# Optimization experiments

Measured on AMD Instinct MI355X. Metric: run time of the kernel, lower is better.

Reference implementation:

```python
import jax, jax.numpy as jnp
import numpy as np

N, T, D, H = 32, 512, 1024, 1024


def setup_inputs() -> dict:
    key = jax.random.key(0)
    k1, k2, k3, k4 = jax.random.split(key, 4)
    x = jax.random.normal(k1, (N, T, D), jnp.float32)
    prev_ht = jax.random.normal(k2, (N, H), jnp.float32)
    # scale weights to keep sigmoid/tanh out of hard saturation
    weight = jax.random.normal(k3, (D + H, 3 * (D + H)), jnp.float32) / np.sqrt(D + H).astype(np.float32)
    bias = jax.random.normal(k4, (3 * (D + H),), jnp.float32) * 0.1
    return {"x": x, "prev_ht": prev_ht, "weight": weight, "bias": bias}


def _gridgru_forward(x, prev_ht, weight, bias):
    # weight layout per get_weights()
    Wxt = weight[:D, :3 * H]          # (D, 3H)
    Wxd = weight[:D, 3 * H:]          # (D, 3D)
    Whd = weight[D:, 3 * H:]          # (H, 3D)
    Whtg = weight[D:, :2 * H]         # (H, 2H)
    Whtc = weight[D:, 2 * H:3 * H]    # (H, H)
    bt = bias[:3 * H]
    bd = bias[3 * H:]

    # input projection for temporal gates, done once: (N, T, 3H)
    gates = jnp.einsum('ntd,dk->ntk', x, Wxt) + bt

    # temporal GRU recurrence over T (zoneout=0, inference)
    def step(h, g):  # h: (N,H), g: (N,3H)
        gg = jax.nn.sigmoid(g[:, :2 * H] + h @ Whtg)
        u = gg[:, :H]
        r = gg[:, H:]
        hc = jnp.tanh(g[:, 2 * H:] + (r * h) @ Whtc)
        hn = h + u * (hc - h)  # = h - u*h + u*hc
        return hn, hn

    last_ht, ht_t = jax.lax.scan(step, prev_ht, jnp.swapaxes(gates, 0, 1))
    ht = jnp.swapaxes(ht_t, 0, 1)  # (N, T, H)

    # depth-wise gated recurrence (applied per-timestep, no sequential dep)
    grd = jax.nn.sigmoid(bd[:2 * D]
                         + jnp.einsum('ntd,de->nte', x, Wxd[:, :2 * D])
                         + jnp.einsum('nth,he->nte', ht, Whd[:, :2 * D]))
    ud = grd[..., :D]
    rd = grd[..., D:]
    hcd = jnp.tanh(bd[2 * D:]
                   + jnp.einsum('nth,he->nte', ht, Whd[:, 2 * D:])
                   + jnp.einsum('ntd,de->nte', rd * x, Wxd[:, 2 * D:]))
    h = x + ud * (hcd - x)  # = x - ud*x + ud*hcd
    return h, last_ht


def reference(x, prev_ht, weight, bias):
    return _gridgru_forward(x, prev_ht, weight, bias)
```

## Files before the change

kernel.cpp:

```cpp
#include <hip/hip_runtime.h>
#include <stdint.h>

#define T_STEPS 512
#define GBLK 64

typedef short short8 __attribute__((ext_vector_type(8)));
typedef float floatx4 __attribute__((ext_vector_type(4)));

__device__ __forceinline__ unsigned short f2bf(float f) {
  unsigned int u = __builtin_bit_cast(unsigned int, f);
  u = u + 0x7fff + ((u >> 16) & 1);
  return (unsigned short)(u >> 16);
}
__device__ __forceinline__ float bf2f(unsigned short s) {
  unsigned int u = ((unsigned int)s) << 16;
  return __builtin_bit_cast(float, u);
}
__device__ __forceinline__ float sigm(float x) { return 1.f / (1.f + __expf(-x)); }
__device__ __forceinline__ float tanh_fast(float x) {
  float e2 = __expf(2.f * x);
  return 1.f - 2.f / (e2 + 1.f);
}

__device__ __forceinline__ void gload16(const void* g, const void* l) {
  __builtin_amdgcn_global_load_lds((const __attribute__((address_space(1))) unsigned int*)g,
                                   (__attribute__((address_space(3))) unsigned int*)l,
                                   16, 0, 0);
}

__global__ void pack_bf(const float* __restrict__ in, unsigned short* __restrict__ out, int n) {
  int i = blockIdx.x * 256 + threadIdx.x;
  if (i < n) out[i] = f2bf(in[i]);
}

__global__ void packT(const float* __restrict__ src, int srcStride,
                      unsigned short* __restrict__ dst, int dldk, int koff) {
  __shared__ float tile[32][33];
  int tx = threadIdx.x, ty = threadIdx.y;
  int e0 = blockIdx.x * 32, k0 = blockIdx.y * 32;
#pragma unroll
  for (int i = 0; i < 4; ++i)
    tile[ty + 8 * i][tx] = src[(size_t)(k0 + ty + 8 * i) * srcStride + e0 + tx];
  __syncthreads();
#pragma unroll
  for (int i = 0; i < 4; ++i)
    dst[(size_t)(e0 + ty + 8 * i) * dldk + koff + k0 + tx] = f2bf(tile[tx][ty + 8 * i]);
}

__global__ void sentinel(float* out, float v) { out[0] = v; }

template <int EPI>
__global__ __launch_bounds__(256) void gemm_bt(
    const unsigned short* __restrict__ A0, const unsigned short* __restrict__ A1,
    const unsigned short* __restrict__ BT,
    int M, int Nn, int K, int KA0,
    const float* __restrict__ bias,
    unsigned short* __restrict__ out_bf,
    const float* __restrict__ xf,
    float* __restrict__ ud,
    unsigned short* __restrict__ rdx,
    float* __restrict__ outf) {
  __shared__ unsigned short At[128 * 32];
  __shared__ unsigned short Bt[128 * 32];
  const int tid = threadIdx.x;
  const int lane = tid & 63, wave = tid >> 6;
  const int wm = wave >> 1, wn = wave & 1;
  const int m0 = blockIdx.y * 128, n0 = blockIdx.x * 128;
  const int lr = lane & 15, lk = (lane >> 4) * 8;
  floatx4 acc[4][4] = {};

  for (int k0 = 0; k0 < K; k0 += 32) {
    const unsigned short* As;
    int kk;
    if (k0 < KA0) { As = A0 + (size_t)m0 * KA0 + k0; kk = KA0; }
    else          { As = A1 + (size_t)m0 * (K - KA0) + (k0 - KA0); kk = K - KA0; }
#pragma unroll
    for (int j = 0; j < 2; ++j) {
      int chunk = j * 256 + tid;
      int row = chunk >> 2, kc = chunk & 3;
      gload16(As + (size_t)row * kk + kc * 8, (const char*)At + chunk * 16);
    }
    const unsigned short* Bs = BT + (size_t)n0 * K + k0;
#pragma unroll
    for (int j = 0; j < 2; ++j) {
      int chunk = j * 256 + tid;
      int row = chunk >> 2, kc = chunk & 3;
      gload16(Bs + (size_t)row * K + kc * 8, (const char*)Bt + chunk * 16);
    }
    __syncthreads();
    short8 a[4], b[4];
#pragma unroll
    for (int i = 0; i < 4; ++i) a[i] = *(const short8*)(At + (wm * 64 + i * 16 + lr) * 32 + lk);
#pragma unroll
    for (int i = 0; i < 4; ++i) b[i] = *(const short8*)(Bt + (wn * 64 + i * 16 + lr) * 32 + lk);
#pragma unroll
    for (int i = 0; i < 4; ++i)
#pragma unroll
      for (int j = 0; j < 4; ++j)
        acc[i][j] = __builtin_amdgcn_mfma_f32_16x16x32_bf16(a[i], b[j], acc[i][j], 0, 0, 0);
    __syncthreads();
  }

#pragma unroll
  for (int i = 0; i < 4; ++i) {
#pragma unroll
    for (int j = 0; j < 4; ++j) {
      int col = n0 + wn * 64 + j * 16 + lr;
#pragma unroll
      for (int r = 0; r < 4; ++r) {
        int row = m0 + wm * 64 + i * 16 + (lane >> 4) * 4 + r;
        float v = acc[i][j][r];
        if constexpr (EPI == 0) {
          out_bf[(size_t)row * Nn + col] = f2bf(v + bias[col]);
        } else if constexpr (EPI == 1) {
          float s = sigm(v + bias[col]);
          if (col < 1024) {
            ud[(size_t)row * 1024 + col] = s;
          } else {
            size_t ix = (size_t)row * 1024 + (col - 1024);
            rdx[ix] = f2bf(s * xf[ix]);
          }
        } else {
          float hc = tanh_fast(v + bias[col]);
          size_t ix = (size_t)row * 1024 + col;
          float xv = xf[ix];
          outf[ix] = xv + ud[ix] * (hc - xv);
        }
      }
    }
  }
}

__device__ __forceinline__ void group_barrier(unsigned int* c) {
  __syncthreads();
  if (threadIdx.x == 0) {
    __hip_atomic_fetch_add(c, 1u, __ATOMIC_RELAXED, __HIP_MEMORY_SCOPE_AGENT);
    int spins = 0;
    while (__hip_atomic_load(c, __ATOMIC_RELAXED, __HIP_MEMORY_SCOPE_AGENT) < (unsigned)GBLK) {
      if (++spins > (1 << 27)) break;
      if (spins > 64) __builtin_amdgcn_s_sleep(2);
    }
    (void)__hip_atomic_load(c, __ATOMIC_ACQUIRE, __HIP_MEMORY_SCOPE_AGENT);
  }
  __syncthreads();
}

__global__ __launch_bounds__(256, 1) void scan_pk(
    const unsigned short* __restrict__ wgT,
    const unsigned short* __restrict__ wcT,
    const unsigned short* __restrict__ gates,
    const float* __restrict__ ph,
    unsigned short* __restrict__ hb,
    unsigned short* __restrict__ rhbuf,
    unsigned short* __restrict__ htb,
    float* __restrict__ lastht,
    unsigned int* __restrict__ bars)
{
  __shared__ unsigned short Wg[32 * 1024];
  __shared__ unsigned short Wc[16 * 1024];
  __shared__ unsigned short Stg[16 * 1024];
  __shared__ float Part[4][16][17];
  __shared__ float Ubuf[16][16];
  __shared__ float Hloc[16][16];
  __shared__ unsigned short Gbuf[3][16][16];

  const int tid = threadIdx.x;
  const int lane = tid & 63, wave = tid >> 6;
  const int lr = lane & 15, lq = lane >> 4;
  const int bid = blockIdx.x;
  const int g = bid >> 6, b = bid & 63;
  const int row0 = g * 16, col0 = b * 16;
  unsigned int* bar = bars + g * 1026;

#pragma unroll
  for (int i = 0; i < 16; ++i) {
    int p = i * 256 + tid;
    int wr = p >> 7, kcp = p & 127;
    int kc = kcp ^ (wr & 7);
    int grow = (wr < 16) ? (col0 + wr) : (1024 + col0 + (wr - 16));
    gload16(wgT + (size_t)grow * 1024 + kc * 8, (const char*)Wg + p * 16);
  }
#pragma unroll
  for (int i = 0; i < 8; ++i) {
    int p = i * 256 + tid;
    int wr = p >> 7, kcp = p & 127;
    int kc = kcp ^ (wr & 7);
    gload16(wcT + (size_t)(col0 + wr) * 1024 + kc * 8, (const char*)Wc + p * 16);
  }
  {
    int r = tid >> 4, c = tid & 15;
    float v = ph[(size_t)(row0 + r) * 1024 + col0 + c];
    Hloc[r][c] = v;
    __hip_atomic_store(&hb[(size_t)(row0 + r) * 1024 + col0 + c], f2bf(v),
                       __ATOMIC_RELAXED, __HIP_MEMORY_SCOPE_AGENT);
  }
  group_barrier(&bar[0]);

  for (int t = 0; t < T_STEPS; ++t) {
#pragma unroll
    for (int i = 0; i < 8; ++i) {
      int p = i * 256 + tid;
      int r = p >> 7, kcp = p & 127;
      int kc = kcp ^ (r & 7);
      gload16(hb + (size_t)(row0 + r) * 1024 + kc * 8, (const char*)Stg + p * 16);
    }
    if (tid < 96) {
      int s = tid >> 5, row = (tid >> 1) & 15, half = tid & 1;
      int gcol = (s == 0) ? col0 : (s == 1) ? (1024 + col0) : (2048 + col0);
      gload16(gates + ((size_t)(row0 + row) * T_STEPS + t) * 3072 + gcol + half * 8,
              (const char*)&Gbuf[0][0][0] + tid * 16);
    }
    __syncthreads();

    {
      const int wc = wave & 1, wk = wave >> 1;
      floatx4 acc = {};
#pragma unroll
      for (int ks = 0; ks < 16; ++ks) {
        int kci = (wk * 16 + ks) * 4 + lq;
        int sw = kci ^ (lr & 7);
        short8 av = *(const short8*)(Stg + lr * 1024 + sw * 8);
        short8 bv = *(const short8*)(Wg + (wc * 16 + lr) * 1024 + sw * 8);
        acc = __builtin_amdgcn_mfma_f32_16x16x32_bf16(av, bv, acc, 0, 0, 0);
      }
      const int tix = wk * 2 + wc;
#pragma unroll
      for (int r = 0; r < 4; ++r) Part[tix][lq * 4 + r][lr] = acc[r];
    }
    __syncthreads();

#pragma unroll
    for (int e = 0; e < 2; ++e) {
      int o = e * 256 + tid;
      int row = o >> 5, col = o & 31;
      int wcc = col >> 4, c = col & 15;
      float sum = Part[wcc][row][c] + Part[2 + wcc][row][c];
      float sv = sigm(sum + bf2f(Gbuf[wcc][row][c]));
      if (wcc == 0) {
        Ubuf[row][c] = sv;
      } else {
        unsigned short rv = f2bf(sv * Hloc[row][c]);
        __hip_atomic_store(&rhbuf[(size_t)(row0 + row) * 1024 + col0 + c], rv,
                           __ATOMIC_RELAXED, __HIP_MEMORY_SCOPE_AGENT);
      }
    }
    group_barrier(&bar[1 + 2 * t]);

#pragma unroll
    for (int i = 0; i < 8; ++i) {
      int p = i * 256 + tid;
      int r = p >> 7, kcp = p & 127;
      int kc = kcp ^ (r & 7);
      gload16(rhbuf + (size_t)(row0 + r) * 1024 + kc * 8, (const char*)Stg + p * 16);
    }
    __syncthreads();

    {
      floatx4 acc = {};
#pragma unroll
      for (int ks = 0; ks < 8; ++ks) {
        int kci = (wave * 8 + ks) * 4 + lq;
        int sw = kci ^ (lr & 7);
        short8 av = *(const short8*)(Stg + lr * 1024 + sw * 8);
        short8 bv = *(const short8*)(Wc + lr * 1024 + sw * 8);
        acc = __builtin_amdgcn_mfma_f32_16x16x32_bf16(av, bv, acc, 0, 0, 0);
      }
#pragma unroll
      for (int r = 0; r < 4; ++r) Part[wave][lq * 4 + r][lr] = acc[r];
    }
    __syncthreads();

    {
      int row = tid >> 4, c = tid & 15;
      float sum = Part[0][row][c] + Part[1][row][c] + Part[2][row][c] + Part[3][row][c];
      float hc = tanh_fast(sum + bf2f(Gbuf[2][row][c]));
      float h = Hloc[row][c], u = Ubuf[row][c];
      float hn = h + u * (hc - h);
      Hloc[row][c] = hn;
      unsigned short hv = f2bf(hn);
      __hip_atomic_store(&hb[(size_t)(row0 + row) * 1024 + col0 + c], hv,
                         __ATOMIC_RELAXED, __HIP_MEMORY_SCOPE_AGENT);
      htb[((size_t)(row0 + row) * T_STEPS + t) * 1024 + col0 + c] = hv;
      if (t == T_STEPS - 1) lastht[(size_t)(row0 + row) * 1024 + col0 + c] = hn;
    }
    group_barrier(&bar[2 + 2 * t]);
  }
}

extern "C" void kernel_launch(void* const* d_in, const int* in_sizes, int n_in,
                              void* d_out, int out_size, void* d_ws, size_t ws_size,
                              hipStream_t stream) {
  const float* x    = (const float*)d_in[0];
  const float* ph   = (const float*)d_in[1];
  const float* wgt  = (const float*)d_in[2];
  const float* bias = (const float*)d_in[3];
  float* out = (float*)d_out;

  const size_t SZ_BARS  = 16384;
  const size_t SZ_XBF   = (size_t)16384 * 1024 * 2;
  const size_t SZ_GATES = (size_t)16384 * 3072 * 2;
  const size_t SZ_HTB   = (size_t)16384 * 1024 * 2;
  const size_t SZ_W     = ((size_t)3072 * 1024 + (size_t)2048 * 2048 +
                           (size_t)1024 * 2048 + (size_t)2048 * 1024 +
                           (size_t)1024 * 1024) * 2;
  const size_t SZ_SMALL = (size_t)(32 * 1024) * (2 + 2);
  const size_t REQUIRED = SZ_BARS + SZ_XBF + SZ_GATES + SZ_HTB + SZ_W + SZ_SMALL;

  if (ws_size < REQUIRED) {
    sentinel<<<1, 1, 0, stream>>>(out, (float)ws_size);
    return;
  }

  char* p = (char*)d_ws;
  unsigned int* bars    = (unsigned int*)p;   p += SZ_BARS;
  unsigned short* xbf   = (unsigned short*)p; p += SZ_XBF;
  unsigned short* gates = (unsigned short*)p;
  unsigned short* rdx   = (unsigned short*)p; p += SZ_GATES;
  unsigned short* htb   = (unsigned short*)p; p += SZ_HTB;
  unsigned short* wxtT  = (unsigned short*)p; p += (size_t)3072 * 1024 * 2;
  unsigned short* w1T   = (unsigned short*)p; p += (size_t)2048 * 2048 * 2;
  unsigned short* w2T   = (unsigned short*)p; p += (size_t)1024 * 2048 * 2;
  unsigned short* wgT   = (unsigned short*)p; p += (size_t)2048 * 1024 * 2;
  unsigned short* wcT   = (unsigned short*)p; p += (size_t)1024 * 1024 * 2;
  unsigned short* hb    = (unsigned short*)p; p += (size_t)32 * 1024 * 2;
  unsigned short* rhbuf = (unsigned short*)p; p += (size_t)32 * 1024 * 2;
  float* udf = out;

  hipMemsetAsync(bars, 0, SZ_BARS, stream);

  dim3 tb(32, 8);
  pack_bf<<<65536, 256, 0, stream>>>(x, xbf, 16384 * 1024);
  packT<<<dim3(96, 32), tb, 0, stream>>>(wgt, 6144, wxtT, 1024, 0);
  packT<<<dim3(64, 64), tb, 0, stream>>>(wgt + 3072, 6144, w1T, 2048, 0);
  packT<<<dim3(32, 32), tb, 0, stream>>>(wgt + (size_t)1024 * 6144 + 5120, 6144, w2T, 2048, 0);
  packT<<<dim3(32, 32), tb, 0, stream>>>(wgt + 5120, 6144, w2T, 2048, 1024);
  packT<<<dim3(64, 32), tb, 0, stream>>>(wgt + (size_t)1024 * 6144, 6144, wgT, 1024, 0);
  packT<<<dim3(32, 32), tb, 0, stream>>>(wgt + (size_t)1024 * 6144 + 2048, 6144, wcT, 1024, 0);

  gemm_bt<0><<<dim3(24, 128), 256, 0, stream>>>(xbf, xbf, wxtT, 16384, 3072, 1024, 1024,
                                                bias, gates, nullptr, nullptr, nullptr, nullptr);

  scan_pk<<<128, 256, 0, stream>>>(wgT, wcT, gates, ph, hb, rhbuf, htb,
                                   out + (size_t)16384 * 1024, bars);

  gemm_bt<1><<<dim3(16, 128), 256, 0, stream>>>(xbf, htb, w1T, 16384, 2048, 2048, 1024,
                                                bias + 3072, nullptr, x, udf, rdx, nullptr);
  gemm_bt<2><<<dim3(8, 128), 256, 0, stream>>>(htb, rdx, w2T, 16384, 1024, 2048, 1024,
                                               bias + 5120, nullptr, x, udf, nullptr, out);
}
```

Measured before the change: 4.015 ms.

## Replace counter barriers with per-block epoch flags and split gate computation

The atomic-counter group barriers in the recurrent scan are replaced by per-block monotonic epoch flags. One wavefront polls all 64 peer flags together with a wave-wide vote. The reset-gate matmul is now computed and published first, and the update-gate matmul runs while peer blocks are still publishing, which moves it off the critical path. The gate-input prefetch is issued before the wait, and the history store goes out after the flag is published. This shortens the serial per-timestep latency, at the cost of more flag polling traffic and tighter reasoning about buffer-reuse ordering across steps.

Result: faster. 3.828 ms (-4.6%).

```diff
diff --git a/kernel.cpp b/kernel.cpp
--- a/kernel.cpp
+++ b/kernel.cpp
@@ -131,16 +131,18 @@
   }
 }
 
-__device__ __forceinline__ void group_barrier(unsigned int* c) {
-  __syncthreads();
-  if (threadIdx.x == 0) {
-    __hip_atomic_fetch_add(c, 1u, __ATOMIC_RELAXED, __HIP_MEMORY_SCOPE_AGENT);
+__device__ __forceinline__ void wait_flags(unsigned int* f, unsigned int target) {
+  if (threadIdx.x < 64) {
+    unsigned int v = __hip_atomic_load(&f[threadIdx.x], __ATOMIC_RELAXED,
+                                       __HIP_MEMORY_SCOPE_AGENT);
     int spins = 0;
-    while (__hip_atomic_load(c, __ATOMIC_RELAXED, __HIP_MEMORY_SCOPE_AGENT) < (unsigned)GBLK) {
-      if (++spins > (1 << 27)) break;
-      if (spins > 64) __builtin_amdgcn_s_sleep(2);
-    }
-    (void)__hip_atomic_load(c, __ATOMIC_ACQUIRE, __HIP_MEMORY_SCOPE_AGENT);
+    while (!__all(v >= target)) {
+      if (++spins > (1 << 22)) break;
+      __builtin_amdgcn_s_sleep(1);
+      v = __hip_atomic_load(&f[threadIdx.x], __ATOMIC_RELAXED,
+                            __HIP_MEMORY_SCOPE_AGENT);
+    }
+    (void)__hip_atomic_load(&f[0], __ATOMIC_ACQUIRE, __HIP_MEMORY_SCOPE_AGENT);
   }
   __syncthreads();
 }
@@ -154,7 +156,7 @@
     unsigned short* __restrict__ rhbuf,
     unsigned short* __restrict__ htb,
     float* __restrict__ lastht,
-    unsigned int* __restrict__ bars)
+    unsigned int* __restrict__ flags)
 {
   __shared__ unsigned short Wg[32 * 1024];
   __shared__ unsigned short Wc[16 * 1024];
@@ -170,7 +172,8 @@
   const int bid = blockIdx.x;
   const int g = bid >> 6, b = bid & 63;
   const int row0 = g * 16, col0 = b * 16;
-  unsigned int* bar = bars + g * 1026;
+  unsigned int* fA = flags + (g * 2 + 0) * 64;
+  unsigned int* fB = flags + (g * 2 + 1) * 64;
 
 #pragma unroll
   for (int i = 0; i < 16; ++i) {
@@ -194,9 +197,19 @@
     __hip_atomic_store(&hb[(size_t)(row0 + r) * 1024 + col0 + c], f2bf(v),
                        __ATOMIC_RELAXED, __HIP_MEMORY_SCOPE_AGENT);
   }
-  group_barrier(&bar[0]);
+  __syncthreads();
+  if (tid == 0)
+    __hip_atomic_store(&fB[b], 1u, __ATOMIC_RELAXED, __HIP_MEMORY_SCOPE_AGENT);
 
   for (int t = 0; t < T_STEPS; ++t) {
+    if (tid < 96) {
+      int s = tid >> 5, row = (tid >> 1) & 15, half = tid & 1;
+      int gcol = (s == 0) ? col0 : (s == 1) ? (1024 + col0) : (2048 + col0);
+      gload16(gates + ((size_t)(row0 + row) * T_STEPS + t) * 3072 + gcol + half * 8,
+              (const char*)&Gbuf[0][0][0] + tid * 16);
+    }
+    wait_flags(fB, t + 1);
+
 #pragma unroll
     for (int i = 0; i < 8; ++i) {
       int p = i * 256 + tid;
@@ -204,47 +217,55 @@
       int kc = kcp ^ (r & 7);
       gload16(hb + (size_t)(row0 + r) * 1024 + kc * 8, (const char*)Stg + p * 16);
     }
-    if (tid < 96) {
-      int s = tid >> 5, row = (tid >> 1) & 15, half = tid & 1;
-      int gcol = (s == 0) ? col0 : (s == 1) ? (1024 + col0) : (2048 + col0);
-      gload16(gates + ((size_t)(row0 + row) * T_STEPS + t) * 3072 + gcol + half * 8,
-              (const char*)&Gbuf[0][0][0] + tid * 16);
-    }
-    __syncthreads();
-
-    {
-      const int wc = wave & 1, wk = wave >> 1;
+    __syncthreads();
+
+    {
       floatx4 acc = {};
 #pragma unroll
-      for (int ks = 0; ks < 16; ++ks) {
-        int kci = (wk * 16 + ks) * 4 + lq;
+      for (int ks8 = 0; ks8 < 8; ++ks8) {
+        int kci = (wave * 8 + ks8) * 4 + lq;
         int sw = kci ^ (lr & 7);
         short8 av = *(const short8*)(Stg + lr * 1024 + sw * 8);
-        short8 bv = *(const short8*)(Wg + (wc * 16 + lr) * 1024 + sw * 8);
+        short8 bv = *(const short8*)(Wg + (16 + lr) * 1024 + sw * 8);
         acc = __builtin_amdgcn_mfma_f32_16x16x32_bf16(av, bv, acc, 0, 0, 0);
       }
-      const int tix = wk * 2 + wc;
-#pragma unroll
-      for (int r = 0; r < 4; ++r) Part[tix][lq * 4 + r][lr] = acc[r];
-    }
-    __syncthreads();
-
-#pragma unroll
-    for (int e = 0; e < 2; ++e) {
-      int o = e * 256 + tid;
-      int row = o >> 5, col = o & 31;
-      int wcc = col >> 4, c = col & 15;
-      float sum = Part[wcc][row][c] + Part[2 + wcc][row][c];
-      float sv = sigm(sum + bf2f(Gbuf[wcc][row][c]));
-      if (wcc == 0) {
-        Ubuf[row][c] = sv;
-      } else {
-        unsigned short rv = f2bf(sv * Hloc[row][c]);
-        __hip_atomic_store(&rhbuf[(size_t)(row0 + row) * 1024 + col0 + c], rv,
-                           __ATOMIC_RELAXED, __HIP_MEMORY_SCOPE_AGENT);
+#pragma unroll
+      for (int r = 0; r < 4; ++r) Part[wave][lq * 4 + r][lr] = acc[r];
+    }
+    __syncthreads();
+    {
+      int row = tid >> 4, c = tid & 15;
+      float sum = Part[0][row][c] + Part[1][row][c] + Part[2][row][c] + Part[3][row][c];
+      float sv = sigm(sum + bf2f(Gbuf[1][row][c]));
+      __hip_atomic_store(&rhbuf[(size_t)(row0 + row) * 1024 + col0 + c],
+                         f2bf(sv * Hloc[row][c]),
+                         __ATOMIC_RELAXED, __HIP_MEMORY_SCOPE_AGENT);
+    }
+    __syncthreads();
+    if (tid == 0)
+      __hip_atomic_store(&fA[b], (unsigned)(t + 1), __ATOMIC_RELAXED,
+                         __HIP_MEMORY_SCOPE_AGENT);
+
+    {
+      floatx4 acc = {};
+#pragma unroll
+      for (int ks8 = 0; ks8 < 8; ++ks8) {
+        int kci = (wave * 8 + ks8) * 4 + lq;
+        int sw = kci ^ (lr & 7);
+        short8 av = *(const short8*)(Stg + lr * 1024 + sw * 8);
+        short8 bv = *(const short8*)(Wg + lr * 1024 + sw * 8);
+        acc = __builtin_amdgcn_mfma_f32_16x16x32_bf16(av, bv, acc, 0, 0, 0);
       }
-    }
-    group_barrier(&bar[1 + 2 * t]);
+#pragma unroll
+      for (int r = 0; r < 4; ++r) Part[wave][lq * 4 + r][lr] = acc[r];
+    }
+    __syncthreads();
+    {
+      int row = tid >> 4, c = tid & 15;
+      float sum = Part[0][row][c] + Part[1][row][c] + Part[2][row][c] + Part[3][row][c];
+      Ubuf[row][c] = sigm(sum + bf2f(Gbuf[0][row][c]));
+    }
+    wait_flags(fA, t + 1);
 
 #pragma unroll
     for (int i = 0; i < 8; ++i) {
@@ -258,8 +279,8 @@
     {
       floatx4 acc = {};
 #pragma unroll
-      for (int ks = 0; ks < 8; ++ks) {
-        int kci = (wave * 8 + ks) * 4 + lq;
+      for (int ks8 = 0; ks8 < 8; ++ks8) {
+        int kci = (wave * 8 + ks8) * 4 + lq;
         int sw = kci ^ (lr & 7);
         short8 av = *(const short8*)(Stg + lr * 1024 + sw * 8);
         short8 bv = *(const short8*)(Wc + lr * 1024 + sw * 8);
@@ -269,21 +290,23 @@
       for (int r = 0; r < 4; ++r) Part[wave][lq * 4 + r][lr] = acc[r];
     }
     __syncthreads();
-
-    {
-      int row = tid >> 4, c = tid & 15;
+    float hn;
+    int row = tid >> 4, c = tid & 15;
+    {
       float sum = Part[0][row][c] + Part[1][row][c] + Part[2][row][c] + Part[3][row][c];
       float hc = tanh_fast(sum + bf2f(Gbuf[2][row][c]));
       float h = Hloc[row][c], u = Ubuf[row][c];
-      float hn = h + u * (hc - h);
+      hn = h + u * (hc - h);
       Hloc[row][c] = hn;
-      unsigned short hv = f2bf(hn);
-      __hip_atomic_store(&hb[(size_t)(row0 + row) * 1024 + col0 + c], hv,
+      __hip_atomic_store(&hb[(size_t)(row0 + row) * 1024 + col0 + c], f2bf(hn),
                          __ATOMIC_RELAXED, __HIP_MEMORY_SCOPE_AGENT);
-      htb[((size_t)(row0 + row) * T_STEPS + t) * 1024 + col0 + c] = hv;
-      if (t == T_STEPS - 1) lastht[(size_t)(row0 + row) * 1024 + col0 + c] = hn;
-    }
-    group_barrier(&bar[2 + 2 * t]);
+    }
+    __syncthreads();
+    if (tid == 0)
+      __hip_atomic_store(&fB[b], (unsigned)(t + 2), __ATOMIC_RELAXED,
+                         __HIP_MEMORY_SCOPE_AGENT);
+    htb[((size_t)(row0 + row) * T_STEPS + t) * 1024 + col0 + c] = f2bf(hn);
+    if (t == T_STEPS - 1) lastht[(size_t)(row0 + row) * 1024 + col0 + c] = hn;
   }
 }
 
@@ -312,7 +335,7 @@
   }
 
   char* p = (char*)d_ws;
-  unsigned int* bars    = (unsigned int*)p;   p += SZ_BARS;
+  unsigned int* flags   = (unsigned int*)p;   p += SZ_BARS;
   unsigned short* xbf   = (unsigned short*)p; p += SZ_XBF;
   unsigned short* gates = (unsigned short*)p;
   unsigned short* rdx   = (unsigned short*)p; p += SZ_GATES;
@@ -326,7 +349,7 @@
   unsigned short* rhbuf = (unsigned short*)p; p += (size_t)32 * 1024 * 2;
   float* udf = out;
 
-  hipMemsetAsync(bars, 0, SZ_BARS, stream);
+  hipMemsetAsync(flags, 0, SZ_BARS, stream);
 
   dim3 tb(32, 8);
   pack_bf<<<65536, 256, 0, stream>>>(x, xbf, 16384 * 1024);
@@ -341,7 +364,7 @@
                                                 bias, gates, nullptr, nullptr, nullptr, nullptr);
 
   scan_pk<<<128, 256, 0, stream>>>(wgT, wcT, gates, ph, hb, rhbuf, htb,
-                                   out + (size_t)16384 * 1024, bars);
+                                   out + (size_t)16384 * 1024, flags);
 
   gemm_bt<1><<<dim3(16, 128), 256, 0, stream>>>(xbf, htb, w1T, 16384, 2048, 2048, 1024,
                                                 bias + 3072, nullptr, x, udf, rdx, nullptr);
```

## Replace counter grid barriers in recurrent scan with per-block flag polling

Applied to the files above, without the earlier changes.

The persistent scan kernel drops its shared atomic-counter group barrier in favour of per-block monotonic flags that all 64 lanes of a wave poll together. Each thread also keeps its hidden state in a register, loads h and r*h straight into registers with cache-bypassing loads instead of staging through LDS, and splits the K reduction across all four waves for both the update and reset gates. The aim is shorter synchronisation latency on each of the 1024 sequential phases. In exchange it depends on the sc0/sc1 store and load coherence, and the bounded spin loop can exit silently on a timeout.

Measured after the change: 5.462 ms. 36.1% more time.

```diff
diff --git a/kernel.cpp b/kernel.cpp
--- a/kernel.cpp
+++ b/kernel.cpp
@@ -2,10 +2,11 @@
 #include <stdint.h>
 
 #define T_STEPS 512
-#define GBLK 64
 
 typedef short short8 __attribute__((ext_vector_type(8)));
 typedef float floatx4 __attribute__((ext_vector_type(4)));
+
+#define MFMA16 __builtin_amdgcn_mfma_f32_16x16x32_bf16
 
 __device__ __forceinline__ unsigned short f2bf(float f) {
   unsigned int u = __builtin_bit_cast(unsigned int, f);
@@ -26,6 +27,29 @@
   __builtin_amdgcn_global_load_lds((const __attribute__((address_space(1))) unsigned int*)g,
                                    (__attribute__((address_space(3))) unsigned int*)l,
                                    16, 0, 0);
+}
+
+__device__ __forceinline__ short8 ld16x(const unsigned short* p) {
+  short8 r;
+  asm volatile("global_load_dwordx4 %0, %1, off sc0 sc1" : "=v"(r) : "v"(p));
+  return r;
+}
+__device__ __forceinline__ void st2x(unsigned short* p, unsigned short v) {
+  unsigned int vv = v;
+  asm volatile("global_store_short %0, %1, off sc0 sc1" :: "v"(p), "v"(vv));
+}
+__device__ __forceinline__ void drain_vm() {
+  asm volatile("s_waitcnt vmcnt(0)" ::: "memory");
+}
+__device__ __forceinline__ void poll_flags(unsigned int* f, unsigned int target) {
+  unsigned int* p = f + (threadIdx.x & 63);
+  int spins = 0;
+  do {
+    unsigned int v = __hip_atomic_load(p, __ATOMIC_RELAXED, __HIP_MEMORY_SCOPE_AGENT);
+    if (__all((int)(v >= target))) break;
+    if (spins > 8) __builtin_amdgcn_s_sleep(1);
+  } while (++spins < (1 << 16));
+  __builtin_amdgcn_sched_barrier(0);
 }
 
 __global__ void pack_bf(const float* __restrict__ in, unsigned short* __restrict__ out, int n) {
@@ -97,7 +121,7 @@
     for (int i = 0; i < 4; ++i)
 #pragma unroll
       for (int j = 0; j < 4; ++j)
-        acc[i][j] = __builtin_amdgcn_mfma_f32_16x16x32_bf16(a[i], b[j], acc[i][j], 0, 0, 0);
+        acc[i][j] = MFMA16(a[i], b[j], acc[i][j], 0, 0, 0);
     __syncthreads();
   }
 
@@ -131,20 +155,6 @@
   }
 }
 
-__device__ __forceinline__ void group_barrier(unsigned int* c) {
-  __syncthreads();
-  if (threadIdx.x == 0) {
-    __hip_atomic_fetch_add(c, 1u, __ATOMIC_RELAXED, __HIP_MEMORY_SCOPE_AGENT);
-    int spins = 0;
-    while (__hip_atomic_load(c, __ATOMIC_RELAXED, __HIP_MEMORY_SCOPE_AGENT) < (unsigned)GBLK) {
-      if (++spins > (1 << 27)) break;
-      if (spins > 64) __builtin_amdgcn_s_sleep(2);
-    }
-    (void)__hip_atomic_load(c, __ATOMIC_ACQUIRE, __HIP_MEMORY_SCOPE_AGENT);
-  }
-  __syncthreads();
-}
-
 __global__ __launch_bounds__(256, 1) void scan_pk(
     const unsigned short* __restrict__ wgT,
     const unsigned short* __restrict__ wcT,
@@ -154,136 +164,131 @@
     unsigned short* __restrict__ rhbuf,
     unsigned short* __restrict__ htb,
     float* __restrict__ lastht,
-    unsigned int* __restrict__ bars)
+    unsigned int* __restrict__ ctl)
 {
-  __shared__ unsigned short Wg[32 * 1024];
+  __shared__ unsigned short Wu[16 * 1024];
+  __shared__ unsigned short Wr[16 * 1024];
   __shared__ unsigned short Wc[16 * 1024];
-  __shared__ unsigned short Stg[16 * 1024];
-  __shared__ float Part[4][16][17];
-  __shared__ float Ubuf[16][16];
-  __shared__ float Hloc[16][16];
-  __shared__ unsigned short Gbuf[3][16][16];
+  __shared__ float Part[8][16][17];
 
   const int tid = threadIdx.x;
   const int lane = tid & 63, wave = tid >> 6;
   const int lr = lane & 15, lq = lane >> 4;
-  const int bid = blockIdx.x;
-  const int g = bid >> 6, b = bid & 63;
+  const int g = blockIdx.x >> 6, b = blockIdx.x & 63;
   const int row0 = g * 16, col0 = b * 16;
-  unsigned int* bar = bars + g * 1026;
-
-#pragma unroll
-  for (int i = 0; i < 16; ++i) {
-    int p = i * 256 + tid;
-    int wr = p >> 7, kcp = p & 127;
-    int kc = kcp ^ (wr & 7);
-    int grow = (wr < 16) ? (col0 + wr) : (1024 + col0 + (wr - 16));
-    gload16(wgT + (size_t)grow * 1024 + kc * 8, (const char*)Wg + p * 16);
-  }
+  const int myrow = tid >> 4, myc = tid & 15;
+  unsigned int* fA = ctl + g * 128;
+  unsigned int* fB = fA + 64;
+
 #pragma unroll
   for (int i = 0; i < 8; ++i) {
     int p = i * 256 + tid;
     int wr = p >> 7, kcp = p & 127;
     int kc = kcp ^ (wr & 7);
-    gload16(wcT + (size_t)(col0 + wr) * 1024 + kc * 8, (const char*)Wc + p * 16);
-  }
-  {
-    int r = tid >> 4, c = tid & 15;
-    float v = ph[(size_t)(row0 + r) * 1024 + col0 + c];
-    Hloc[r][c] = v;
-    __hip_atomic_store(&hb[(size_t)(row0 + r) * 1024 + col0 + c], f2bf(v),
-                       __ATOMIC_RELAXED, __HIP_MEMORY_SCOPE_AGENT);
-  }
-  group_barrier(&bar[0]);
+    gload16(wgT + (size_t)(col0 + wr) * 1024 + kc * 8,          (const char*)Wu + p * 16);
+    gload16(wgT + (size_t)(1024 + col0 + wr) * 1024 + kc * 8,   (const char*)Wr + p * 16);
+    gload16(wcT + (size_t)(col0 + wr) * 1024 + kc * 8,          (const char*)Wc + p * 16);
+  }
+
+  float Hl = ph[(size_t)(row0 + myrow) * 1024 + col0 + myc];
+  st2x(&hb[(size_t)(row0 + myrow) * 1024 + col0 + myc], f2bf(Hl));
+  drain_vm();
+  __syncthreads();
+  if (tid == 0)
+    __hip_atomic_store(&fB[b], 1u, __ATOMIC_RELAXED, __HIP_MEMORY_SCOPE_AGENT);
 
   for (int t = 0; t < T_STEPS; ++t) {
-#pragma unroll
-    for (int i = 0; i < 8; ++i) {
-      int p = i * 256 + tid;
-      int r = p >> 7, kcp = p & 127;
-      int kc = kcp ^ (r & 7);
-      gload16(hb + (size_t)(row0 + r) * 1024 + kc * 8, (const char*)Stg + p * 16);
-    }
-    if (tid < 96) {
-      int s = tid >> 5, row = (tid >> 1) & 15, half = tid & 1;
-      int gcol = (s == 0) ? col0 : (s == 1) ? (1024 + col0) : (2048 + col0);
-      gload16(gates + ((size_t)(row0 + row) * T_STEPS + t) * 3072 + gcol + half * 8,
-              (const char*)&Gbuf[0][0][0] + tid * 16);
-    }
-    __syncthreads();
-
-    {
-      const int wc = wave & 1, wk = wave >> 1;
-      floatx4 acc = {};
-#pragma unroll
-      for (int ks = 0; ks < 16; ++ks) {
-        int kci = (wk * 16 + ks) * 4 + lq;
-        int sw = kci ^ (lr & 7);
-        short8 av = *(const short8*)(Stg + lr * 1024 + sw * 8);
-        short8 bv = *(const short8*)(Wg + (wc * 16 + lr) * 1024 + sw * 8);
-        acc = __builtin_amdgcn_mfma_f32_16x16x32_bf16(av, bv, acc, 0, 0, 0);
+    size_t gbase = ((size_t)(row0 + myrow) * T_STEPS + t) * 3072 + col0 + myc;
+    unsigned short gU = gates[gbase];
+    unsigned short gR = gates[gbase + 1024];
+    unsigned short gC = gates[gbase + 2048];
+
+    poll_flags(fB, (unsigned)(t + 1));
+
+    short8 av[8];
+    {
+      const unsigned short* hsrc = hb + (size_t)(row0 + lr) * 1024 + wave * 256 + lq * 8;
+#pragma unroll
+      for (int kc = 0; kc < 8; ++kc) av[kc] = ld16x(hsrc + kc * 32);
+    }
+    drain_vm();
+    __builtin_amdgcn_sched_barrier(0);
+
+    {
+      floatx4 aR = {}, aU = {};
+#pragma unroll
+      for (int kc = 0; kc < 8; ++kc) {
+        int ch = (wave * 32 + kc * 4 + lq) ^ (lr & 7);
+        short8 bR = *(const short8*)(Wr + lr * 1024 + ch * 8);
+        short8 bU = *(const short8*)(Wu + lr * 1024 + ch * 8);
+        aR = MFMA16(av[kc], bR, aR, 0, 0, 0);
+        aU = MFMA16(av[kc], bU, aU, 0, 0, 0);
       }
-      const int tix = wk * 2 + wc;
-#pragma unroll
-      for (int r = 0; r < 4; ++r) Part[tix][lq * 4 + r][lr] = acc[r];
-    }
-    __syncthreads();
-
-#pragma unroll
-    for (int e = 0; e < 2; ++e) {
-      int o = e * 256 + tid;
-      int row = o >> 5, col = o & 31;
-      int wcc = col >> 4, c = col & 15;
-      float sum = Part[wcc][row][c] + Part[2 + wcc][row][c];
-      float sv = sigm(sum + bf2f(Gbuf[wcc][row][c]));
-      if (wcc == 0) {
-        Ubuf[row][c] = sv;
-      } else {
-        unsigned short rv = f2bf(sv * Hloc[row][c]);
-        __hip_atomic_store(&rhbuf[(size_t)(row0 + row) * 1024 + col0 + c], rv,
-                           __ATOMIC_RELAXED, __HIP_MEMORY_SCOPE_AGENT);
+#pragma unroll
+      for (int r = 0; r < 4; ++r) {
+        Part[wave][lq * 4 + r][lr] = aR[r];
+        Part[4 + wave][lq * 4 + r][lr] = aU[r];
       }
     }
-    group_barrier(&bar[1 + 2 * t]);
-
-#pragma unroll
-    for (int i = 0; i < 8; ++i) {
-      int p = i * 256 + tid;
-      int r = p >> 7, kcp = p & 127;
-      int kc = kcp ^ (r & 7);
-      gload16(rhbuf + (size_t)(row0 + r) * 1024 + kc * 8, (const char*)Stg + p * 16);
-    }
-    __syncthreads();
-
-    {
-      floatx4 acc = {};
-#pragma unroll
-      for (int ks = 0; ks < 8; ++ks) {
-        int kci = (wave * 8 + ks) * 4 + lq;
-        int sw = kci ^ (lr & 7);
-        short8 av = *(const short8*)(Stg + lr * 1024 + sw * 8);
-        short8 bv = *(const short8*)(Wc + lr * 1024 + sw * 8);
-        acc = __builtin_amdgcn_mfma_f32_16x16x32_bf16(av, bv, acc, 0, 0, 0);
+    __syncthreads();
+    float uv;
+    {
+      float rpre = Part[0][myrow][myc] + Part[1][myrow][myc] +
+                   Part[2][myrow][myc] + Part[3][myrow][myc];
+      float upre = Part[4][myrow][myc] + Part[5][myrow][myc] +
+                   Part[6][myrow][myc] + Part[7][myrow][myc];
+      float rv = sigm(rpre + bf2f(gR));
+      uv = sigm(upre + bf2f(gU));
+      st2x(&rhbuf[(size_t)(row0 + myrow) * 1024 + col0 + myc], f2bf(rv * Hl));
+    }
+    drain_vm();
+    __syncthreads();
+    if (tid == 0)
+      __hip_atomic_store(&fA[b], (unsigned)(t + 1), __ATOMIC_RELAXED,
+                         __HIP_MEMORY_SCOPE_AGENT);
+
+    poll_flags(fA, (unsigned)(t + 1));
+
+    short8 av2[8];
+    {
+      const unsigned short* rsrc = rhbuf + (size_t)(row0 + lr) * 1024 + wave * 256 + lq * 8;
+#pragma unroll
+      for (int kc = 0; kc < 8; ++kc) av2[kc] = ld16x(rsrc + kc * 32);
+    }
+    drain_vm();
+    __builtin_amdgcn_sched_barrier(0);
+
+    {
+      floatx4 c0 = {}, c1 = {};
+#pragma unroll
+      for (int kc = 0; kc < 8; kc += 2) {
+        int ch0 = (wave * 32 + kc * 4 + lq) ^ (lr & 7);
+        int ch1 = (wave * 32 + (kc + 1) * 4 + lq) ^ (lr & 7);
+        short8 b0 = *(const short8*)(Wc + lr * 1024 + ch0 * 8);
+        short8 b1 = *(const short8*)(Wc + lr * 1024 + ch1 * 8);
+        c0 = MFMA16(av2[kc], b0, c0, 0, 0, 0);
+        c1 = MFMA16(av2[kc + 1], b1, c1, 0, 0, 0);
       }
 #pragma unroll
-      for (int r = 0; r < 4; ++r) Part[wave][lq * 4 + r][lr] = acc[r];
-    }
-    __syncthreads();
-
-    {
-      int row = tid >> 4, c = tid & 15;
-      float sum = Part[0][row][c] + Part[1][row][c] + Part[2][row][c] + Part[3][row][c];
-      float hc = tanh_fast(sum + bf2f(Gbuf[2][row][c]));
-      float h = Hloc[row][c], u = Ubuf[row][c];
-      float hn = h + u * (hc - h);
-      Hloc[row][c] = hn;
+      for (int r = 0; r < 4; ++r) Part[wave][lq * 4 + r][lr] = c0[r] + c1[r];
+    }
+    __syncthreads();
+    {
+      float cpre = Part[0][myrow][myc] + Part[1][myrow][myc] +
+                   Part[2][myrow][myc] + Part[3][myrow][myc];
+      float hc = tanh_fast(cpre + bf2f(gC));
+      float hn = Hl + uv * (hc - Hl);
+      Hl = hn;
       unsigned short hv = f2bf(hn);
-      __hip_atomic_store(&hb[(size_t)(row0 + row) * 1024 + col0 + c], hv,
-                         __ATOMIC_RELAXED, __HIP_MEMORY_SCOPE_AGENT);
-      htb[((size_t)(row0 + row) * T_STEPS + t) * 1024 + col0 + c] = hv;
-      if (t == T_STEPS - 1) lastht[(size_t)(row0 + row) * 1024 + col0 + c] = hn;
-    }
-    group_barrier(&bar[2 + 2 * t]);
+      st2x(&hb[(size_t)(row0 + myrow) * 1024 + col0 + myc], hv);
+      htb[((size_t)(row0 + myrow) * T_STEPS + t) * 1024 + col0 + myc] = hv;
+      if (t == T_STEPS - 1) lastht[(size_t)(row0 + myrow) * 1024 + col0 + myc] = hn;
+    }
+    drain_vm();
+    __syncthreads();
+    if (tid == 0)
+      __hip_atomic_store(&fB[b], (unsigned)(t + 2), __ATOMIC_RELAXED,
+                         __HIP_MEMORY_SCOPE_AGENT);
   }
 }
 
@@ -296,7 +301,7 @@
   const float* bias = (const float*)d_in[3];
   float* out = (float*)d_out;
 
-  const size_t SZ_BARS  = 16384;
+  const size_t SZ_CTL   = 16384;
   const size_t SZ_XBF   = (size_t)16384 * 1024 * 2;
   const size_t SZ_GATES = (size_t)16384 * 3072 * 2;
   const size_t SZ_HTB   = (size_t)16384 * 1024 * 2;
@@ -304,7 +309,7 @@
                            (size_t)1024 * 2048 + (size_t)2048 * 1024 +
                            (size_t)1024 * 1024) * 2;
   const size_t SZ_SMALL = (size_t)(32 * 1024) * (2 + 2);
-  const size_t REQUIRED = SZ_BARS + SZ_XBF + SZ_GATES + SZ_HTB + SZ_W + SZ_SMALL;
+  const size_t REQUIRED = SZ_CTL + SZ_XBF + SZ_GATES + SZ_HTB + SZ_W + SZ_SMALL;
 
   if (ws_size < REQUIRED) {
     sentinel<<<1, 1, 0, stream>>>(out, (float)ws_size);
@@ -312,7 +317,7 @@
   }
 
   char* p = (char*)d_ws;
-  unsigned int* bars    = (unsigned int*)p;   p += SZ_BARS;
+  unsigned int* ctl     = (unsigned int*)p;   p += SZ_CTL;
   unsigned short* xbf   = (unsigned short*)p; p += SZ_XBF;
   unsigned short* gates = (unsigned short*)p;
   unsigned short* rdx   = (unsigned short*)p; p += SZ_GATES;
@@ -326,7 +331,7 @@
   unsigned short* rhbuf = (unsigned short*)p; p += (size_t)32 * 1024 * 2;
   float* udf = out;
 
-  hipMemsetAsync(bars, 0, SZ_BARS, stream);
+  hipMemsetAsync(ctl, 0, SZ_CTL, stream);
 
   dim3 tb(32, 8);
   pack_bf<<<65536, 256, 0, stream>>>(x, xbf, 16384 * 1024);
@@ -341,7 +346,7 @@
                                                 bias, gates, nullptr, nullptr, nullptr, nullptr);
 
   scan_pk<<<128, 256, 0, stream>>>(wgT, wcT, gates, ph, hb, rhbuf, htb,
-                                   out + (size_t)16384 * 1024, bars);
+                                   out + (size_t)16384 * 1024, ctl);
 
   gemm_bt<1><<<dim3(16, 128), 256, 0, stream>>>(xbf, htb, w1T, 16384, 2048, 2048, 1024,
                                                 bias + 3072, nullptr, x, udf, rdx, nullptr);
```
